# Kernel optimization log

Hardware: AMD Instinct MI355X
Metric: run time of the kernel (lower is better)

## Reference

```python
import jax, jax.numpy as jnp
import numpy as np

N_M, N_H = 50000, 50000
E = 600000
D_IN, D_OUT = 128, 128
LN_EPS = 1e-5
NORM_EPS = 1e-12


def _segment_mean(x, seg, n):
    # PyG 'mean' aggregation: sum / count, 0 for isolated nodes (count clamped to 1)
    s = jax.ops.segment_sum(x, seg, num_segments=n)
    c = jax.ops.segment_sum(jnp.ones((seg.shape[0], 1), x.dtype), seg, num_segments=n)
    return s / jnp.maximum(c, 1.0)


def _sage(t_src, t_dst, ei, Wl, bl, Wr):
    # SAGEConv: lin_l(mean_j x_j) + lin_r(x_i), then L2-normalize rows
    agg = _segment_mean(t_src[ei[0]], ei[1], t_dst.shape[0])
    out = agg @ Wl + bl + t_dst @ Wr
    nrm = jnp.maximum(jnp.linalg.norm(out, axis=-1, keepdims=True), NORM_EPS)
    return out / nrm


def _layer_norm(x, g, b):
    mu = jnp.mean(x, axis=-1, keepdims=True)
    v = jnp.var(x, axis=-1, keepdims=True)
    return (x - mu) / jnp.sqrt(v + LN_EPS) * g + b


def setup_inputs() -> dict:
    key = jax.random.key(0)
    ks = jax.random.split(key, 24)
    r = lambda i, shape: jax.random.normal(ks[i], shape, dtype=jnp.float32) * 0.05
    inp = {
        'x_microbe': jax.random.normal(ks[0], (N_M, D_IN), dtype=jnp.float32),
        'x_host': jax.random.normal(ks[1], (N_H, D_IN), dtype=jnp.float32),
        # per-node-type linear transforms
        'W_nt_m': r(2, (D_IN, D_OUT)), 'b_nt_m': r(3, (D_OUT,)),
        'W_nt_h': r(4, (D_IN, D_OUT)), 'b_nt_h': r(5, (D_OUT,)),
        # SAGEConv params per edge type (lin_l has bias, lin_r has no bias)
        'Wl_mm': r(6, (D_OUT, D_OUT)), 'bl_mm': r(7, (D_OUT,)), 'Wr_mm': r(8, (D_OUT, D_OUT)),
        'Wl_mh': r(9, (D_OUT, D_OUT)), 'bl_mh': r(10, (D_OUT,)), 'Wr_mh': r(11, (D_OUT, D_OUT)),
        'Wl_hm': r(12, (D_OUT, D_OUT)), 'bl_hm': r(13, (D_OUT,)), 'Wr_hm': r(14, (D_OUT, D_OUT)),
        # LayerNorm affine params per node type
        'g_m': jnp.ones((D_OUT,), jnp.float32), 'be_m': jnp.zeros((D_OUT,), jnp.float32),
        'g_h': jnp.ones((D_OUT,), jnp.float32), 'be_h': jnp.zeros((D_OUT,), jnp.float32),
        # edge indices [2, E]: row0 = src, row1 = dst
        'ei_mm': jax.random.randint(ks[15], (2, E), 0, N_M, dtype=jnp.int32),
        'ei_mh': jnp.stack([jax.random.randint(ks[16], (E,), 0, N_M, dtype=jnp.int32),
                            jax.random.randint(ks[17], (E,), 0, N_H, dtype=jnp.int32)]),
        'ei_hm': jnp.stack([jax.random.randint(ks[18], (E,), 0, N_H, dtype=jnp.int32),
                            jax.random.randint(ks[19], (E,), 0, N_M, dtype=jnp.int32)]),
    }
    return inp


def reference(x_microbe, x_host, W_nt_m, b_nt_m, W_nt_h, b_nt_h,
              Wl_mm, bl_mm, Wr_mm, Wl_mh, bl_mh, Wr_mh, Wl_hm, bl_hm, Wr_hm,
              g_m, be_m, g_h, be_h, ei_mm, ei_mh, ei_hm):
    # per-type linear transforms
    t_m = x_microbe @ W_nt_m + b_nt_m
    t_h = x_host @ W_nt_h + b_nt_h
    # SAGEConv per edge type
    o_mm = _sage(t_m, t_m, ei_mm, Wl_mm, bl_mm, Wr_mm)  # microbe -> microbe
    o_mh = _sage(t_m, t_h, ei_mh, Wl_mh, bl_mh, Wr_mh)  # microbe -> host
    o_hm = _sage(t_h, t_m, ei_hm, Wl_hm, bl_hm, Wr_hm)  # host -> microbe
    # HeteroConv aggr='mean' over edge types per dst node type
    conv_m = 0.5 * (o_mm + o_hm)
    conv_h = o_mh
    # residual + LayerNorm (dropout is identity in eval mode)
    out_m = _layer_norm(t_m + conv_m, g_m, be_m)
    out_h = _layer_norm(t_h + conv_h, g_h, be_h)
    return out_m, out_h
```

## Files before the change

### kernel.cpp

```cpp
#include <hip/hip_runtime.h>

typedef unsigned short u16;
typedef unsigned int u32;
typedef __attribute__((ext_vector_type(8))) short bf16x8;
typedef __attribute__((ext_vector_type(4))) float f32x4;

#define LDSN 13312
#define CHUNK 16384

__device__ __forceinline__ float bf_lo(u32 u){ return __uint_as_float(u << 16); }
__device__ __forceinline__ float bf_hi(u32 u){ return __uint_as_float(u & 0xffff0000u); }
__device__ __forceinline__ float bf2f(u16 v){ return __uint_as_float((u32)v << 16); }
__device__ __forceinline__ u16 f2bf(float f){
    u32 u = __float_as_uint(f);
    u32 r = (u + 0x7fffu + ((u >> 16) & 1u)) >> 16;
    return (u16)r;
}
__device__ __forceinline__ u32 pack2(float a, float b){
    return (u32)f2bf(a) | ((u32)f2bf(b) << 16);
}

__global__ __launch_bounds__(256) void prep_kernel(
    const float* __restrict__ Wf0, const float* __restrict__ Wf1,
    const float* __restrict__ Wf2, const float* __restrict__ Wf3,
    const float* __restrict__ Wf4, const float* __restrict__ Wf5,
    u16* __restrict__ WF,
    const float* __restrict__ Xm, const float* __restrict__ Wm,
    const float* __restrict__ bm, u16* __restrict__ Tm, int NM,
    const float* __restrict__ Xh, const float* __restrict__ Wh,
    const float* __restrict__ bh, u16* __restrict__ Th, int NH,
    int gm, int gh)
{
    int bid = blockIdx.x;
    if (bid < 6){
        const float* W = bid == 0 ? Wf0 : bid == 1 ? Wf1 : bid == 2 ? Wf2 :
                         bid == 3 ? Wf3 : bid == 4 ? Wf4 : Wf5;
        u16* dst = WF + (size_t)bid * 16384;
        #pragma unroll 4
        for (int k = 0; k < 64; ++k){
            int i = k * 256 + threadIdx.x;
            int j   = i & 7;
            int l16 = (i >> 3) & 15;
            int qd  = (i >> 7) & 3;
            int q   = (i >> 9) & 3;
            int tt  = (i >> 11) & 1;
            int w   = (i >> 12) & 3;
            dst[i] = f2bf(W[(q * 32 + qd * 8 + j) * 128 + (w * 32 + tt * 16 + l16)]);
        }
        return;
    }
    bid -= 6;
    const float *A, *W, *bias; u16* C; int N, lgrid, lbid;
    if (bid < gm){ A = Xm; W = Wm; bias = bm; C = Tm; N = NM; lgrid = gm; lbid = bid; }
    else         { A = Xh; W = Wh; bias = bh; C = Th; N = NH; lgrid = gh; lbid = bid - gm; }

    int tid = threadIdx.x;
    int wave = tid >> 6, lane = tid & 63;
    int colHalf = wave & 1;
    int ln16 = lane & 15, quad = lane >> 4;

    bf16x8 Bfrag[4][4];
    #pragma unroll
    for (int t = 0; t < 4; ++t){
        int col = colHalf * 64 + t * 16 + ln16;
        #pragma unroll
        for (int q = 0; q < 4; ++q){
            bf16x8 f;
            #pragma unroll
            for (int j = 0; j < 8; ++j)
                f[j] = (short)f2bf(W[(q * 32 + quad * 8 + j) * 128 + col]);
            Bfrag[t][q] = f;
        }
    }
    float bv[4];
    #pragma unroll
    for (int t = 0; t < 4; ++t)
        bv[t] = bias[colHalf * 64 + t * 16 + ln16];

    int rowBlocks = (N + 15) >> 4;
    for (int rb = lbid * 2 + (wave >> 1); rb < rowBlocks; rb += lgrid * 2){
        int row0 = rb * 16;
        int ar = row0 + ln16; if (ar > N - 1) ar = N - 1;
        const float* Arow = A + (size_t)ar * 128 + quad * 8;
        bf16x8 Af[4];
        #pragma unroll
        for (int q = 0; q < 4; ++q){
            f32x4 lo = *(const f32x4*)(Arow + q * 32);
            f32x4 hi = *(const f32x4*)(Arow + q * 32 + 4);
            bf16x8 f;
            #pragma unroll
            for (int j = 0; j < 4; ++j){ f[j] = (short)f2bf(lo[j]); f[4+j] = (short)f2bf(hi[j]); }
            Af[q] = f;
        }
        f32x4 acc[4];
        #pragma unroll
        for (int t = 0; t < 4; ++t) acc[t] = (f32x4){bv[t], bv[t], bv[t], bv[t]};
        #pragma unroll
        for (int q = 0; q < 4; ++q)
            #pragma unroll
            for (int t = 0; t < 4; ++t)
                acc[t] = __builtin_amdgcn_mfma_f32_16x16x32_bf16(Af[q], Bfrag[t][q], acc[t], 0, 0, 0);
        #pragma unroll
        for (int t = 0; t < 4; ++t){
            int col = colHalf * 64 + t * 16 + ln16;
            #pragma unroll
            for (int r = 0; r < 4; ++r){
                int row = row0 + quad * 4 + r;
                if (row < N) C[(size_t)row * 128 + col] = f2bf(acc[t][r]);
            }
        }
    }
}

__global__ __launch_bounds__(256) void histL_kernel(
    const int* __restrict__ d0, const int* __restrict__ d1, const int* __restrict__ d2,
    u16* __restrict__ rk0, u16* __restrict__ rk1, u16* __restrict__ rk2,
    int E0, int E1, int E2, int n0, int n1, int n2,
    int c0, int c1, int c2, int R0, int R1, int R2,
    u16* __restrict__ C0, u16* __restrict__ C1, u16* __restrict__ C2)
{
    __shared__ u32 lc[LDSN];
    int bid = blockIdx.x;
    const int* dp; u16 *rk, *cp; int E, n, cc, rr;
    if (bid < c0 * R0){ dp = d0; rk = rk0; cp = C0; E = E0; n = n0; cc = bid / R0; rr = bid % R0; }
    else if (bid < c0 * R0 + c1 * R1){ int l = bid - c0 * R0; dp = d1; rk = rk1; cp = C1; E = E1; n = n1; cc = l / R1; rr = l % R1; }
    else { int l = bid - c0 * R0 - c1 * R1; dp = d2; rk = rk2; cp = C2; E = E2; n = n2; cc = l / R2; rr = l % R2; }
    for (int i = threadIdx.x; i < LDSN; i += 256) lc[i] = 0;
    __syncthreads();
    int r0 = rr * LDSN, r1 = min(r0 + LDSN, n);
    int i0 = cc * CHUNK, i1 = min(i0 + CHUNK, E);
    for (int i = i0 + threadIdx.x; i < i1; i += 256){
        int x = dp[i];
        if ((unsigned)x < (unsigned)n && x >= r0 && x < r1)
            rk[i] = (u16)atomicAdd(&lc[x - r0], 1u);
    }
    __syncthreads();
    u16* op = cp + (size_t)cc * n;
    for (int x = r0 + threadIdx.x; x < r1; x += 256) op[x] = (u16)lc[x - r0];
}

__global__ __launch_bounds__(256) void scan_blocks_kernel(
    const u16* __restrict__ C0, const u16* __restrict__ C1, const u16* __restrict__ C2,
    int c0, int c1, int c2, int NM, int NH, int n,
    int* __restrict__ off, int* __restrict__ part)
{
    __shared__ int lds[256];
    int tid = threadIdx.x;
    int base = blockIdx.x * 2048 + tid * 8;
    int v[8]; int s = 0;
    #pragma unroll
    for (int j = 0; j < 8; ++j){
        int idx = base + j;
        int tot = 0;
        if (idx < n){
            const u16* cp; int ch, w, x;
            if (idx < NM){ cp = C0; ch = c0; w = NM; x = idx; }
            else if (idx < 2 * NM){ cp = C1; ch = c1; w = NM; x = idx - NM; }
            else { cp = C2; ch = c2; w = NH; x = idx - 2 * NM; }
            for (int cc = 0; cc < ch; ++cc) tot += cp[(size_t)cc * w + x];
        }
        v[j] = s; s += tot;
    }
    lds[tid] = s;
    __syncthreads();
    for (int d = 1; d < 256; d <<= 1){
        int t = (tid >= d) ? lds[tid - d] : 0;
        __syncthreads();
        lds[tid] += t;
        __syncthreads();
    }
    int thrBase = (tid > 0) ? lds[tid - 1] : 0;
    if (tid == 255) part[blockIdx.x] = lds[255];
    #pragma unroll
    for (int j = 0; j < 8; ++j){
        int idx = base + j;
        if (idx < n) off[idx] = thrBase + v[j];
    }
}

__global__ __launch_bounds__(128) void scan_part_kernel(
    int* __restrict__ part, int np, int* __restrict__ total_slot)
{
    __shared__ int lds[128];
    int tid = threadIdx.x;
    lds[tid] = (tid < np) ? part[tid] : 0;
    __syncthreads();
    for (int d = 1; d < 128; d <<= 1){
        int t = (tid >= d) ? lds[tid - d] : 0;
        __syncthreads();
        lds[tid] += t;
        __syncthreads();
    }
    if (tid < np) part[tid] = (tid > 0) ? lds[tid - 1] : 0;
    if (tid == 0) *total_slot = lds[np - 1 < 0 ? 0 : np - 1];
}

__global__ __launch_bounds__(256) void colbase_kernel(
    const u16* __restrict__ C0, const u16* __restrict__ C1, const u16* __restrict__ C2,
    int* __restrict__ B0, int* __restrict__ B1, int* __restrict__ B2,
    int c0, int c1, int c2, int NM, int NH, int n,
    int* __restrict__ off, const int* __restrict__ part)
{
    int idx = blockIdx.x * 256 + threadIdx.x;
    if (idx >= n) return;
    int run = off[idx] + part[idx >> 11];
    off[idx] = run;
    const u16* cp; int* bp; int ch, w, x;
    if (idx < NM){ cp = C0; bp = B0; ch = c0; w = NM; x = idx; }
    else if (idx < 2 * NM){ cp = C1; bp = B1; ch = c1; w = NM; x = idx - NM; }
    else { cp = C2; bp = B2; ch = c2; w = NH; x = idx - 2 * NM; }
    for (int cc = 0; cc < ch; ++cc){
        bp[(size_t)cc * w + x] = run;
        run += cp[(size_t)cc * w + x];
    }
}

__global__ __launch_bounds__(256) void fill3_kernel(
    const int* __restrict__ s0, const int* __restrict__ s1, const int* __restrict__ s2,
    const int* __restrict__ d0, const int* __restrict__ d1, const int* __restrict__ d2,
    const u16* __restrict__ rk0, const u16* __restrict__ rk1, const u16* __restrict__ rk2,
    int E0, int E1, int E2, int n0, int n1, int n2,
    const int* __restrict__ B0, const int* __restrict__ B1, const int* __restrict__ B2,
    int* __restrict__ slot)
{
    int t = blockIdx.y;
    const int* sp = t == 0 ? s0 : (t == 1 ? s1 : s2);
    const int* dp = t == 0 ? d0 : (t == 1 ? d1 : d2);
    const u16* rk = t == 0 ? rk0 : (t == 1 ? rk1 : rk2);
    const int* bp = t == 0 ? B0 : (t == 1 ? B1 : B2);
    int E = t == 0 ? E0 : (t == 1 ? E1 : E2);
    int n = t == 0 ? n0 : (t == 1 ? n1 : n2);
    int base = blockIdx.x * 1024 + threadIdx.x;
    #pragma unroll
    for (int k = 0; k < 4; ++k){
        int i = base + k * 256;
        if (i < E){
            int x = dp[i];
            if ((unsigned)x < (unsigned)n){
                int cc = i / CHUNK;
                slot[bp[(size_t)cc * n + x] + (int)rk[i]] = sp[i];
            }
        }
    }
}

__global__ __launch_bounds__(256) void gather3_kernel(
    const u16* __restrict__ TM, const u16* __restrict__ TH,
    const int* __restrict__ off, const int* __restrict__ slot,
    u32* __restrict__ AGGM, u32* __restrict__ AGGH, int NM, int NH)
{
    int n3 = 2 * NM + NH;
    int wid = (int)((blockIdx.x * 256u + threadIdx.x) >> 6);
    int lane = threadIdx.x & 63;
    int nw = (gridDim.x * 256) >> 6;

    for (int id = wid; id < n3; id += nw){
        int b = off[id], e = off[id + 1];
        int deg = e - b;
        const u16* Tsrc; int nsrc;
        if (id < NM){ Tsrc = TM; nsrc = NM; }
        else if (id < 2 * NM){ Tsrc = TH; nsrc = NH; }
        else { Tsrc = TM; nsrc = NM; }

        int take = deg < 64 ? deg : 64;
        int ms = 0;
        if (lane < take){
            ms = slot[b + lane];
            if ((unsigned)ms >= (unsigned)nsrc) ms = 0;
        }

        float a0=0.f,a1=0.f,b0f=0.f,b1f=0.f,c0=0.f,c1=0.f,d0f=0.f,d1f=0.f;
        float e0=0.f,e1=0.f,f0=0.f,f1=0.f,g0=0.f,g1=0.f,h0=0.f,h1=0.f;
        int j = 0;
        for (; j + 8 <= take; j += 8){
            int i0 = __shfl(ms, j);     int i1 = __shfl(ms, j + 1);
            int i2 = __shfl(ms, j + 2); int i3 = __shfl(ms, j + 3);
            int i4 = __shfl(ms, j + 4); int i5 = __shfl(ms, j + 5);
            int i6 = __shfl(ms, j + 6); int i7 = __shfl(ms, j + 7);
            u32 u0 = *(const u32*)(Tsrc + (size_t)i0 * 128 + lane * 2);
            u32 u1 = *(const u32*)(Tsrc + (size_t)i1 * 128 + lane * 2);
            u32 u2 = *(const u32*)(Tsrc + (size_t)i2 * 128 + lane * 2);
            u32 u3 = *(const u32*)(Tsrc + (size_t)i3 * 128 + lane * 2);
            u32 u4 = *(const u32*)(Tsrc + (size_t)i4 * 128 + lane * 2);
            u32 u5 = *(const u32*)(Tsrc + (size_t)i5 * 128 + lane * 2);
            u32 u6 = *(const u32*)(Tsrc + (size_t)i6 * 128 + lane * 2);
            u32 u7 = *(const u32*)(Tsrc + (size_t)i7 * 128 + lane * 2);
            a0 += bf_lo(u0); a1 += bf_hi(u0);
            b0f += bf_lo(u1); b1f += bf_hi(u1);
            c0 += bf_lo(u2); c1 += bf_hi(u2);
            d0f += bf_lo(u3); d1f += bf_hi(u3);
            e0 += bf_lo(u4); e1 += bf_hi(u4);
            f0 += bf_lo(u5); f1 += bf_hi(u5);
            g0 += bf_lo(u6); g1 += bf_hi(u6);
            h0 += bf_lo(u7); h1 += bf_hi(u7);
        }
        for (; j + 4 <= take; j += 4){
            int i0 = __shfl(ms, j);     int i1 = __shfl(ms, j + 1);
            int i2 = __shfl(ms, j + 2); int i3 = __shfl(ms, j + 3);
            u32 u0 = *(const u32*)(Tsrc + (size_t)i0 * 128 + lane * 2);
            u32 u1 = *(const u32*)(Tsrc + (size_t)i1 * 128 + lane * 2);
            u32 u2 = *(const u32*)(Tsrc + (size_t)i2 * 128 + lane * 2);
            u32 u3 = *(const u32*)(Tsrc + (size_t)i3 * 128 + lane * 2);
            a0 += bf_lo(u0); a1 += bf_hi(u0);
            b0f += bf_lo(u1); b1f += bf_hi(u1);
            c0 += bf_lo(u2); c1 += bf_hi(u2);
            d0f += bf_lo(u3); d1f += bf_hi(u3);
        }
        for (; j < take; ++j){
            int i0 = __shfl(ms, j);
            u32 u0 = *(const u32*)(Tsrc + (size_t)i0 * 128 + lane * 2);
            a0 += bf_lo(u0); a1 += bf_hi(u0);
        }
        for (int j2 = b + 64; j2 < e; ++j2){
            int i0 = slot[j2];
            if ((unsigned)i0 >= (unsigned)nsrc) i0 = 0;
            u32 u0 = *(const u32*)(Tsrc + (size_t)i0 * 128 + lane * 2);
            a0 += bf_lo(u0); a1 += bf_hi(u0);
        }
        float s0 = ((a0 + b0f) + (c0 + d0f)) + ((e0 + f0) + (g0 + h0));
        float s1 = ((a1 + b1f) + (c1 + d1f)) + ((e1 + f1) + (g1 + h1));
        float inv = 1.0f / (float)(deg < 1 ? 1 : deg);
        u32 pv = pack2(s0 * inv, s1 * inv);
        if (id < 2 * NM) AGGM[(size_t)id * 64 + lane] = pv;
        else             AGGH[(size_t)(id - 2 * NM) * 64 + lane] = pv;
    }
}

template<int NT>
__global__ __launch_bounds__(256) void gemmln_kernel(
    const u32* __restrict__ AG1, const u32* __restrict__ AG2,
    const u16* __restrict__ Tdst,
    const u16* __restrict__ WFl1, const u16* __restrict__ WFr1, const float* __restrict__ bl1,
    const u16* __restrict__ WFl2, const u16* __restrict__ WFr2, const float* __restrict__ bl2,
    const float* __restrict__ g, const float* __restrict__ be,
    float* __restrict__ outp, int N, float scale)
{
    __shared__ float redN[NT][4][16];
    __shared__ float redS[2][4][16];

    int tid = threadIdx.x;
    int wave = tid >> 6, lane = tid & 63;
    int ln16 = lane & 15, quad = lane >> 4;

    const u32* AG[2] = {AG1, AG2};
    const u16* WFl[2] = {WFl1, WFl2};
    const u16* WFr[2] = {WFr1, WFr2};
    const float* bls[2] = {bl1, bl2};

    bf16x8 BL[NT][2][4], BR[NT][2][4];
    float bv[NT][2];
    #pragma unroll
    for (int et = 0; et < NT; ++et){
        #pragma unroll
        for (int t = 0; t < 2; ++t){
            bv[et][t] = bls[et][wave * 32 + t * 16 + ln16];
            #pragma unroll
            for (int q = 0; q < 4; ++q){
                int fo = ((((wave * 2 + t) * 4 + q) * 4 + quad) * 16 + ln16) * 8;
                BL[et][t][q] = *(const bf16x8*)(WFl[et] + fo);
                BR[et][t][q] = *(const bf16x8*)(WFr[et] + fo);
            }
        }
    }
    float gv[2], bev[2];
    #pragma unroll
    for (int t = 0; t < 2; ++t){
        int col = wave * 32 + t * 16 + ln16;
        gv[t] = g[col]; bev[t] = be[col];
    }

    int tiles = (N + 15) >> 4;
    for (int tile = blockIdx.x; tile < tiles; tile += gridDim.x){
        int row0 = tile * 16;
        int ar = row0 + ln16; if (ar > N - 1) ar = N - 1;
        const u16* Ar2 = Tdst + (size_t)ar * 128 + quad * 8;

        f32x4 acc[NT][2];
        #pragma unroll
        for (int et = 0; et < NT; ++et)
            #pragma unroll
            for (int t = 0; t < 2; ++t)
                acc[et][t] = (f32x4){bv[et][t], bv[et][t], bv[et][t], bv[et][t]};

        #pragma unroll
        for (int q = 0; q < 4; ++q){
            bf16x8 afr = *(const bf16x8*)(Ar2 + q * 32);
            #pragma unroll
            for (int et = 0; et < NT; ++et){
                bf16x8 afl = *(const bf16x8*)(AG[et] + (size_t)ar * 64 + q * 16 + quad * 4);
                #pragma unroll
                for (int t = 0; t < 2; ++t){
                    acc[et][t] = __builtin_amdgcn_mfma_f32_16x16x32_bf16(afl, BL[et][t][q], acc[et][t], 0, 0, 0);
                    acc[et][t] = __builtin_amdgcn_mfma_f32_16x16x32_bf16(afr, BR[et][t][q], acc[et][t], 0, 0, 0);
                }
            }
        }

        #pragma unroll
        for (int et = 0; et < NT; ++et){
            #pragma unroll
            for (int r = 0; r < 4; ++r){
                float s = acc[et][0][r] * acc[et][0][r] + acc[et][1][r] * acc[et][1][r];
                #pragma unroll
                for (int m = 1; m < 16; m <<= 1) s += __shfl_xor(s, m);
                if (ln16 == 0) redN[et][wave][quad * 4 + r] = s;
            }
        }
        __syncthreads();

        float yv[2][4];
        float lsum[4], lsq[4];
        #pragma unroll
        for (int r = 0; r < 4; ++r){
            int r16 = quad * 4 + r;
            int row = row0 + r16;
            int crow = row < N ? row : N - 1;
            float sc[NT];
            #pragma unroll
            for (int et = 0; et < NT; ++et){
                float tot = redN[et][0][r16] + redN[et][1][r16] + redN[et][2][r16] + redN[et][3][r16];
                sc[et] = scale / fmaxf(sqrtf(tot), 1e-12f);
            }
            float s1v = 0.f, s2v = 0.f;
            #pragma unroll
            for (int t = 0; t < 2; ++t){
                int col = wave * 32 + t * 16 + ln16;
                float y = bf2f(Tdst[(size_t)crow * 128 + col]);
                #pragma unroll
                for (int et = 0; et < NT; ++et) y += acc[et][t][r] * sc[et];
                yv[t][r] = y;
                s1v += y; s2v += y * y;
            }
            #pragma unroll
            for (int m = 1; m < 16; m <<= 1){ s1v += __shfl_xor(s1v, m); s2v += __shfl_xor(s2v, m); }
            lsum[r] = s1v; lsq[r] = s2v;
        }
        if (ln16 == 0){
            #pragma unroll
            for (int r = 0; r < 4; ++r){
                redS[0][wave][quad * 4 + r] = lsum[r];
                redS[1][wave][quad * 4 + r] = lsq[r];
            }
        }
        __syncthreads();

        #pragma unroll
        for (int r = 0; r < 4; ++r){
            int r16 = quad * 4 + r;
            int row = row0 + r16;
            if (row >= N) continue;
            float S1 = redS[0][0][r16] + redS[0][1][r16] + redS[0][2][r16] + redS[0][3][r16];
            float S2 = redS[1][0][r16] + redS[1][1][r16] + redS[1][2][r16] + redS[1][3][r16];
            float mean = S1 * (1.0f / 128.0f);
            float var = S2 * (1.0f / 128.0f) - mean * mean;
            float rstd = rsqrtf(var + 1e-5f);
            #pragma unroll
            for (int t = 0; t < 2; ++t){
                int col = wave * 32 + t * 16 + ln16;
                outp[(size_t)row * 128 + col] = (yv[t][r] - mean) * rstd * gv[t] + bev[t];
            }
        }
        __syncthreads();
    }
}

extern "C" void kernel_launch(void* const* d_in, const int* in_sizes, int n_in,
                              void* d_out, int out_size, void* d_ws, size_t ws_size,
                              hipStream_t stream) {
    const float* xm    = (const float*)d_in[0];
    const float* xh    = (const float*)d_in[1];
    const float* Wnt_m = (const float*)d_in[2];  const float* bnt_m = (const float*)d_in[3];
    const float* Wnt_h = (const float*)d_in[4];  const float* bnt_h = (const float*)d_in[5];
    const float* Wl_mm = (const float*)d_in[6];  const float* bl_mm = (const float*)d_in[7];
    const float* Wr_mm = (const float*)d_in[8];
    const float* Wl_mh = (const float*)d_in[9];  const float* bl_mh = (const float*)d_in[10];
    const float* Wr_mh = (const float*)d_in[11];
    const float* Wl_hm = (const float*)d_in[12]; const float* bl_hm = (const float*)d_in[13];
    const float* Wr_hm = (const float*)d_in[14];
    const float* g_m   = (const float*)d_in[15]; const float* be_m  = (const float*)d_in[16];
    const float* g_h   = (const float*)d_in[17]; const float* be_h  = (const float*)d_in[18];
    const int* ei_mm = (const int*)d_in[19];
    const int* ei_mh = (const int*)d_in[20];
    const int* ei_hm = (const int*)d_in[21];

    const int D = 128;
    const int NM = in_sizes[0] / D;
    const int NH = in_sizes[1] / D;
    const int E1 = in_sizes[19] / 2;
    const int E2 = in_sizes[20] / 2;
    const int E3 = in_sizes[21] / 2;
    const int Esum = E1 + E2 + E3;
    const int n3 = 2 * NM + NH;

    const int c0 = (E1 + CHUNK - 1) / CHUNK;
    const int c1 = (E3 + CHUNK - 1) / CHUNK;
    const int c2 = (E2 + CHUNK - 1) / CHUNK;
    const int R0 = (NM + LDSN - 1) / LDSN;
    const int R1 = (NM + LDSN - 1) / LDSN;
    const int R2 = (NH + LDSN - 1) / LDSN;
    const int HB2 = c0 * R0 + c1 * R1 + c2 * R2;

    char* ws = (char*)d_ws;
    size_t woff = 0;
    auto alloc = [&](size_t bytes) -> void* {
        void* p = ws + woff;
        woff += (bytes + 255) & ~(size_t)255;
        return p;
    };
    u16* T_M   = (u16*)alloc((size_t)NM * D * 2);
    u16* T_H   = (u16*)alloc((size_t)NH * D * 2);
    u16* CNT16 = (u16*)alloc(((size_t)(c0 + c1) * NM + (size_t)c2 * NH) * 2);
    int* OFF3  = (int*)alloc((size_t)(n3 + 1) * 4);
    int* SLOT3 = (int*)alloc((size_t)Esum * 4);
    int* PART  = (int*)alloc(1024 * 4);
    u16* WF    = (u16*)alloc((size_t)6 * 16384 * 2);
    u32* AGGM  = (u32*)alloc((size_t)2 * NM * 64 * 4);
    if (woff > ws_size) return;

    u16* C0p = CNT16;
    u16* C1p = C0p + (size_t)c0 * NM;
    u16* C2p = C1p + (size_t)c1 * NM;

    int* B0p = (int*)d_out;
    int* B1p = B0p + (size_t)c0 * NM;
    int* B2p = B1p + (size_t)c1 * NM;
    u16* RK  = (u16*)(B2p + (size_t)c2 * NH);
    u16* rk0 = RK, *rk1 = RK + E1, *rk2 = RK + E1 + E3;
    u32* AGGH = (u32*)d_out;

    float* OUT_M = (float*)d_out;
    float* OUT_H = (float*)d_out + (size_t)NM * D;

    const int gm = 1024, gh = 1024;
    const int scanBlocks = (n3 + 2047) / 2048;
    int Emax = E1 > E2 ? E1 : E2; if (E3 > Emax) Emax = E3;
    const dim3 egrid((Emax + 1023) / 1024, 3);

    prep_kernel<<<6 + gm + gh, 256, 0, stream>>>(
        Wl_mm, Wr_mm, Wl_hm, Wr_hm, Wl_mh, Wr_mh, WF,
        xm, Wnt_m, bnt_m, T_M, NM,
        xh, Wnt_h, bnt_h, T_H, NH, gm, gh);

    histL_kernel<<<HB2, 256, 0, stream>>>(
        ei_mm + E1, ei_hm + E3, ei_mh + E2,
        rk0, rk1, rk2,
        E1, E3, E2, NM, NM, NH,
        c0, c1, c2, R0, R1, R2,
        C0p, C1p, C2p);

    scan_blocks_kernel<<<scanBlocks, 256, 0, stream>>>(
        C0p, C1p, C2p, c0, c1, c2, NM, NH, n3, OFF3, PART);
    scan_part_kernel<<<1, 128, 0, stream>>>(PART, scanBlocks, OFF3 + n3);
    colbase_kernel<<<(n3 + 255) / 256, 256, 0, stream>>>(
        C0p, C1p, C2p, B0p, B1p, B2p, c0, c1, c2, NM, NH, n3, OFF3, PART);

    fill3_kernel<<<egrid, 256, 0, stream>>>(
        ei_mm, ei_hm, ei_mh,
        ei_mm + E1, ei_hm + E3, ei_mh + E2,
        rk0, rk1, rk2,
        E1, E3, E2, NM, NM, NH,
        B0p, B1p, B2p, SLOT3);

    gather3_kernel<<<2048, 256, 0, stream>>>(
        T_M, T_H, OFF3, SLOT3, AGGM, AGGH, NM, NH);

    gemmln_kernel<1><<<1024, 256, 0, stream>>>(
        AGGH, nullptr, T_H,
        WF + 4 * 16384, WF + 5 * 16384, bl_mh,
        nullptr, nullptr, nullptr,
        g_h, be_h, OUT_H, NH, 1.0f);
    gemmln_kernel<2><<<1024, 256, 0, stream>>>(
        AGGM, AGGM + (size_t)NM * 64, T_M,
        WF + 0 * 16384, WF + 1 * 16384, bl_mm,
        WF + 2 * 16384, WF + 3 * 16384, bl_hm,
        g_m, be_m, OUT_M, NM, 0.5f);
}
```

Measured before the change: 473.3 us.

## Fuse histogram into prep kernel, pack LDS counters, batch gather node loads

Merges the destination-histogram kernel into the weight/linear prep kernel as extra blocks. Both ran before the scan, so one launch now covers them and they can overlap. The LDS counters are packed as two 16-bit values per word to halve shared memory, which may allow more blocks per CU. The gather kernel now has each wave take four nodes, prefetching their offsets and slot indices up front to hide index-load latency. The cost is extra register pressure, and a 16-bit counter would carry into its neighbour if a chunk held 65536 or more hits for one node.

```diff
diff --git a/kernel.cpp b/kernel.cpp
--- a/kernel.cpp
+++ b/kernel.cpp
@@ -20,7 +20,12 @@
     return (u32)f2bf(a) | ((u32)f2bf(b) << 16);
 }
 
-__global__ __launch_bounds__(256) void prep_kernel(
+__global__ __launch_bounds__(256) void fusedA_kernel(
+    const int* __restrict__ d0, const int* __restrict__ d1, const int* __restrict__ d2,
+    u16* __restrict__ rk0, u16* __restrict__ rk1, u16* __restrict__ rk2,
+    int E0, int E1, int E2, int n0, int n1, int n2,
+    int c0, int c1, int c2, int R0, int R1, int R2,
+    u16* __restrict__ C0, u16* __restrict__ C1, u16* __restrict__ C2, int HB2,
     const float* __restrict__ Wf0, const float* __restrict__ Wf1,
     const float* __restrict__ Wf2, const float* __restrict__ Wf3,
     const float* __restrict__ Wf4, const float* __restrict__ Wf5,
@@ -31,7 +36,35 @@
     const float* __restrict__ bh, u16* __restrict__ Th, int NH,
     int gm, int gh)
 {
+    __shared__ u32 lc[LDSN / 2];
     int bid = blockIdx.x;
+    if (bid < HB2){
+        const int* dp; u16 *rk, *cp; int E, n, cc, rr;
+        if (bid < c0 * R0){ dp = d0; rk = rk0; cp = C0; E = E0; n = n0; cc = bid / R0; rr = bid % R0; }
+        else if (bid < c0 * R0 + c1 * R1){ int l = bid - c0 * R0; dp = d1; rk = rk1; cp = C1; E = E1; n = n1; cc = l / R1; rr = l % R1; }
+        else { int l = bid - c0 * R0 - c1 * R1; dp = d2; rk = rk2; cp = C2; E = E2; n = n2; cc = l / R2; rr = l % R2; }
+        for (int i = threadIdx.x; i < LDSN / 2; i += 256) lc[i] = 0;
+        __syncthreads();
+        int r0 = rr * LDSN, r1 = min(r0 + LDSN, n);
+        int i0 = cc * CHUNK, i1 = min(i0 + CHUNK, E);
+        for (int i = i0 + threadIdx.x; i < i1; i += 256){
+            int x = dp[i];
+            if ((unsigned)x < (unsigned)n && x >= r0 && x < r1){
+                int lx = x - r0;
+                int sh = (lx & 1) << 4;
+                u32 old = atomicAdd(&lc[lx >> 1], 1u << sh);
+                rk[i] = (u16)((old >> sh) & 0xffffu);
+            }
+        }
+        __syncthreads();
+        u16* op = cp + (size_t)cc * n;
+        for (int x = r0 + threadIdx.x; x < r1; x += 256){
+            int lx = x - r0;
+            op[x] = (u16)((lc[lx >> 1] >> ((lx & 1) << 4)) & 0xffffu);
+        }
+        return;
+    }
+    bid -= HB2;
     if (bid < 6){
         const float* W = bid == 0 ? Wf0 : bid == 1 ? Wf1 : bid == 2 ? Wf2 :
                          bid == 3 ? Wf3 : bid == 4 ? Wf4 : Wf5;
@@ -112,33 +145,6 @@
     }
 }
 
-__global__ __launch_bounds__(256) void histL_kernel(
-    const int* __restrict__ d0, const int* __restrict__ d1, const int* __restrict__ d2,
-    u16* __restrict__ rk0, u16* __restrict__ rk1, u16* __restrict__ rk2,
-    int E0, int E1, int E2, int n0, int n1, int n2,
-    int c0, int c1, int c2, int R0, int R1, int R2,
-    u16* __restrict__ C0, u16* __restrict__ C1, u16* __restrict__ C2)
-{
-    __shared__ u32 lc[LDSN];
-    int bid = blockIdx.x;
-    const int* dp; u16 *rk, *cp; int E, n, cc, rr;
-    if (bid < c0 * R0){ dp = d0; rk = rk0; cp = C0; E = E0; n = n0; cc = bid / R0; rr = bid % R0; }
-    else if (bid < c0 * R0 + c1 * R1){ int l = bid - c0 * R0; dp = d1; rk = rk1; cp = C1; E = E1; n = n1; cc = l / R1; rr = l % R1; }
-    else { int l = bid - c0 * R0 - c1 * R1; dp = d2; rk = rk2; cp = C2; E = E2; n = n2; cc = l / R2; rr = l % R2; }
-    for (int i = threadIdx.x; i < LDSN; i += 256) lc[i] = 0;
-    __syncthreads();
-    int r0 = rr * LDSN, r1 = min(r0 + LDSN, n);
-    int i0 = cc * CHUNK, i1 = min(i0 + CHUNK, E);
-    for (int i = i0 + threadIdx.x; i < i1; i += 256){
-        int x = dp[i];
-        if ((unsigned)x < (unsigned)n && x >= r0 && x < r1)
-            rk[i] = (u16)atomicAdd(&lc[x - r0], 1u);
-    }
-    __syncthreads();
-    u16* op = cp + (size_t)cc * n;
-    for (int x = r0 + threadIdx.x; x < r1; x += 256) op[x] = (u16)lc[x - r0];
-}
-
 __global__ __launch_bounds__(256) void scan_blocks_kernel(
     const u16* __restrict__ C0, const u16* __restrict__ C1, const u16* __restrict__ C2,
     int c0, int c1, int c2, int NM, int NH, int n,
@@ -254,75 +260,91 @@
     int lane = threadIdx.x & 63;
     int nw = (gridDim.x * 256) >> 6;
 
-    for (int id = wid; id < n3; id += nw){
-        int b = off[id], e = off[id + 1];
-        int deg = e - b;
-        const u16* Tsrc; int nsrc;
-        if (id < NM){ Tsrc = TM; nsrc = NM; }
-        else if (id < 2 * NM){ Tsrc = TH; nsrc = NH; }
-        else { Tsrc = TM; nsrc = NM; }
-
-        int take = deg < 64 ? deg : 64;
-        int ms = 0;
-        if (lane < take){
-            ms = slot[b + lane];
-            if ((unsigned)ms >= (unsigned)nsrc) ms = 0;
-        }
-
-        float a0=0.f,a1=0.f,b0f=0.f,b1f=0.f,c0=0.f,c1=0.f,d0f=0.f,d1f=0.f;
-        float e0=0.f,e1=0.f,f0=0.f,f1=0.f,g0=0.f,g1=0.f,h0=0.f,h1=0.f;
-        int j = 0;
-        for (; j + 8 <= take; j += 8){
-            int i0 = __shfl(ms, j);     int i1 = __shfl(ms, j + 1);
-            int i2 = __shfl(ms, j + 2); int i3 = __shfl(ms, j + 3);
-            int i4 = __shfl(ms, j + 4); int i5 = __shfl(ms, j + 5);
-            int i6 = __shfl(ms, j + 6); int i7 = __shfl(ms, j + 7);
-            u32 u0 = *(const u32*)(Tsrc + (size_t)i0 * 128 + lane * 2);
-            u32 u1 = *(const u32*)(Tsrc + (size_t)i1 * 128 + lane * 2);
-            u32 u2 = *(const u32*)(Tsrc + (size_t)i2 * 128 + lane * 2);
-            u32 u3 = *(const u32*)(Tsrc + (size_t)i3 * 128 + lane * 2);
-            u32 u4 = *(const u32*)(Tsrc + (size_t)i4 * 128 + lane * 2);
-            u32 u5 = *(const u32*)(Tsrc + (size_t)i5 * 128 + lane * 2);
-            u32 u6 = *(const u32*)(Tsrc + (size_t)i6 * 128 + lane * 2);
-            u32 u7 = *(const u32*)(Tsrc + (size_t)i7 * 128 + lane * 2);
-            a0 += bf_lo(u0); a1 += bf_hi(u0);
-            b0f += bf_lo(u1); b1f += bf_hi(u1);
-            c0 += bf_lo(u2); c1 += bf_hi(u2);
-            d0f += bf_lo(u3); d1f += bf_hi(u3);
-            e0 += bf_lo(u4); e1 += bf_hi(u4);
-            f0 += bf_lo(u5); f1 += bf_hi(u5);
-            g0 += bf_lo(u6); g1 += bf_hi(u6);
-            h0 += bf_lo(u7); h1 += bf_hi(u7);
-        }
-        for (; j + 4 <= take; j += 4){
-            int i0 = __shfl(ms, j);     int i1 = __shfl(ms, j + 1);
-            int i2 = __shfl(ms, j + 2); int i3 = __shfl(ms, j + 3);
-            u32 u0 = *(const u32*)(Tsrc + (size_t)i0 * 128 + lane * 2);
-            u32 u1 = *(const u32*)(Tsrc + (size_t)i1 * 128 + lane * 2);
-            u32 u2 = *(const u32*)(Tsrc + (size_t)i2 * 128 + lane * 2);
-            u32 u3 = *(const u32*)(Tsrc + (size_t)i3 * 128 + lane * 2);
-            a0 += bf_lo(u0); a1 += bf_hi(u0);
-            b0f += bf_lo(u1); b1f += bf_hi(u1);
-            c0 += bf_lo(u2); c1 += bf_hi(u2);
-            d0f += bf_lo(u3); d1f += bf_hi(u3);
-        }
-        for (; j < take; ++j){
-            int i0 = __shfl(ms, j);
-            u32 u0 = *(const u32*)(Tsrc + (size_t)i0 * 128 + lane * 2);
-            a0 += bf_lo(u0); a1 += bf_hi(u0);
-        }
-        for (int j2 = b + 64; j2 < e; ++j2){
-            int i0 = slot[j2];
-            if ((unsigned)i0 >= (unsigned)nsrc) i0 = 0;
-            u32 u0 = *(const u32*)(Tsrc + (size_t)i0 * 128 + lane * 2);
-            a0 += bf_lo(u0); a1 += bf_hi(u0);
-        }
-        float s0 = ((a0 + b0f) + (c0 + d0f)) + ((e0 + f0) + (g0 + h0));
-        float s1 = ((a1 + b1f) + (c1 + d1f)) + ((e1 + f1) + (g1 + h1));
-        float inv = 1.0f / (float)(deg < 1 ? 1 : deg);
-        u32 pv = pack2(s0 * inv, s1 * inv);
-        if (id < 2 * NM) AGGM[(size_t)id * 64 + lane] = pv;
-        else             AGGH[(size_t)(id - 2 * NM) * 64 + lane] = pv;
+    for (int id0 = wid * 4; id0 < n3; id0 += nw * 4){
+        int bb[4], dg[4], tk[4], ms[4], ns[4];
+        const u16* Ts[4];
+        #pragma unroll
+        for (int r = 0; r < 4; ++r){
+            int id = id0 + r;
+            int b = 0, e = 0;
+            if (id < n3){ b = off[id]; e = off[id + 1]; }
+            bb[r] = b;
+            int deg = e - b; dg[r] = deg;
+            int take = deg < 64 ? deg : 64; tk[r] = take;
+            const u16* Tsrc; int nsrc;
+            if (id < NM){ Tsrc = TM; nsrc = NM; }
+            else if (id < 2 * NM){ Tsrc = TH; nsrc = NH; }
+            else { Tsrc = TM; nsrc = NM; }
+            Ts[r] = Tsrc; ns[r] = nsrc;
+            int s = 0;
+            if (lane < take){
+                s = slot[b + lane];
+                if ((unsigned)s >= (unsigned)nsrc) s = 0;
+            }
+            ms[r] = s;
+        }
+
+        #pragma unroll
+        for (int r = 0; r < 4; ++r){
+            int id = id0 + r;
+            if (id >= n3) break;
+            const u16* Tsrc = Ts[r];
+            int take = tk[r];
+            float a0=0.f,a1=0.f,b0f=0.f,b1f=0.f,c0=0.f,c1=0.f,d0f=0.f,d1f=0.f;
+            float e0=0.f,e1=0.f,f0=0.f,f1=0.f,g0=0.f,g1=0.f,h0=0.f,h1=0.f;
+            int j = 0;
+            for (; j + 8 <= take; j += 8){
+                int i0 = __shfl(ms[r], j);     int i1 = __shfl(ms[r], j + 1);
+                int i2 = __shfl(ms[r], j + 2); int i3 = __shfl(ms[r], j + 3);
+                int i4 = __shfl(ms[r], j + 4); int i5 = __shfl(ms[r], j + 5);
+                int i6 = __shfl(ms[r], j + 6); int i7 = __shfl(ms[r], j + 7);
+                u32 u0 = *(const u32*)(Tsrc + (size_t)i0 * 128 + lane * 2);
+                u32 u1 = *(const u32*)(Tsrc + (size_t)i1 * 128 + lane * 2);
+                u32 u2 = *(const u32*)(Tsrc + (size_t)i2 * 128 + lane * 2);
+                u32 u3 = *(const u32*)(Tsrc + (size_t)i3 * 128 + lane * 2);
+                u32 u4 = *(const u32*)(Tsrc + (size_t)i4 * 128 + lane * 2);
+                u32 u5 = *(const u32*)(Tsrc + (size_t)i5 * 128 + lane * 2);
+                u32 u6 = *(const u32*)(Tsrc + (size_t)i6 * 128 + lane * 2);
+                u32 u7 = *(const u32*)(Tsrc + (size_t)i7 * 128 + lane * 2);
+                a0 += bf_lo(u0); a1 += bf_hi(u0);
+                b0f += bf_lo(u1); b1f += bf_hi(u1);
+                c0 += bf_lo(u2); c1 += bf_hi(u2);
+                d0f += bf_lo(u3); d1f += bf_hi(u3);
+                e0 += bf_lo(u4); e1 += bf_hi(u4);
+                f0 += bf_lo(u5); f1 += bf_hi(u5);
+                g0 += bf_lo(u6); g1 += bf_hi(u6);
+                h0 += bf_lo(u7); h1 += bf_hi(u7);
+            }
+            for (; j + 4 <= take; j += 4){
+                int i0 = __shfl(ms[r], j);     int i1 = __shfl(ms[r], j + 1);
+                int i2 = __shfl(ms[r], j + 2); int i3 = __shfl(ms[r], j + 3);
+                u32 u0 = *(const u32*)(Tsrc + (size_t)i0 * 128 + lane * 2);
+                u32 u1 = *(const u32*)(Tsrc + (size_t)i1 * 128 + lane * 2);
+                u32 u2 = *(const u32*)(Tsrc + (size_t)i2 * 128 + lane * 2);
+                u32 u3 = *(const u32*)(Tsrc + (size_t)i3 * 128 + lane * 2);
+                a0 += bf_lo(u0); a1 += bf_hi(u0);
+                b0f += bf_lo(u1); b1f += bf_hi(u1);
+                c0 += bf_lo(u2); c1 += bf_hi(u2);
+                d0f += bf_lo(u3); d1f += bf_hi(u3);
+            }
+            for (; j < take; ++j){
+                int i0 = __shfl(ms[r], j);
+                u32 u0 = *(const u32*)(Tsrc + (size_t)i0 * 128 + lane * 2);
+                a0 += bf_lo(u0); a1 += bf_hi(u0);
+            }
+            for (int j2 = bb[r] + 64; j2 < bb[r] + dg[r]; ++j2){
+                int i0 = slot[j2];
+                if ((unsigned)i0 >= (unsigned)ns[r]) i0 = 0;
+                u32 u0 = *(const u32*)(Tsrc + (size_t)i0 * 128 + lane * 2);
+                a0 += bf_lo(u0); a1 += bf_hi(u0);
+            }
+            float s0 = ((a0 + b0f) + (c0 + d0f)) + ((e0 + f0) + (g0 + h0));
+            float s1 = ((a1 + b1f) + (c1 + d1f)) + ((e1 + f1) + (g1 + h1));
+            float inv = 1.0f / (float)(dg[r] < 1 ? 1 : dg[r]);
+            u32 pv = pack2(s0 * inv, s1 * inv);
+            if (id < 2 * NM) AGGM[(size_t)id * 64 + lane] = pv;
+            else             AGGH[(size_t)(id - 2 * NM) * 64 + lane] = pv;
+        }
     }
 }
 
@@ -536,17 +558,15 @@
     int Emax = E1 > E2 ? E1 : E2; if (E3 > Emax) Emax = E3;
     const dim3 egrid((Emax + 1023) / 1024, 3);
 
-    prep_kernel<<<6 + gm + gh, 256, 0, stream>>>(
-        Wl_mm, Wr_mm, Wl_hm, Wr_hm, Wl_mh, Wr_mh, WF,
-        xm, Wnt_m, bnt_m, T_M, NM,
-        xh, Wnt_h, bnt_h, T_H, NH, gm, gh);
-
-    histL_kernel<<<HB2, 256, 0, stream>>>(
+    fusedA_kernel<<<HB2 + 6 + gm + gh, 256, 0, stream>>>(
         ei_mm + E1, ei_hm + E3, ei_mh + E2,
         rk0, rk1, rk2,
         E1, E3, E2, NM, NM, NH,
         c0, c1, c2, R0, R1, R2,
-        C0p, C1p, C2p);
+        C0p, C1p, C2p, HB2,
+        Wl_mm, Wr_mm, Wl_hm, Wr_hm, Wl_mh, Wr_mh, WF,
+        xm, Wnt_m, bnt_m, T_M, NM,
+        xh, Wnt_h, bnt_h, T_H, NH, gm, gh);
 
     scan_blocks_kernel<<<scanBlocks, 256, 0, stream>>>(
         C0p, C1p, C2p, c0, c1, c2, NM, NH, n3, OFF3, PART);
```

Result: faster. 455.5 us (-3.8%).
